# Kernel tuning notes

Hardware: AMD Instinct MI355X
Metric: run time of the kernel (lower is better)

Reference implementation:

```python
import jax, jax.numpy as jnp
import numpy as np

# BD-format field offsets (within 512-dim token vector)
MARK_AX = 0
OP_MUL = 1
OPCODE_BASE = 2          # opcode 27 lives at index OPCODE_BASE + 27
ALU_LO, ALU_HI = 64, 80          # 16-way one-hot nibbles
AX_CARRY_LO, AX_CARRY_HI = 96, 112
OUTPUT_LO, OUTPUT_HI = 128, 144
# GenericE slot layout (within 160-dim GE vector)
NIB_A, NIB_B, RESULT, OP_START = 0, 1, 2, 3
GE_DIM = 160
N_POS = 8
N_LAYERS = 7
OPCODE = 27


def setup_inputs() -> dict:
    key = jax.random.key(0)
    k1, k2, k3 = jax.random.split(key, 3)
    x_bd = jax.random.uniform(k1, (4, 8192, 512), dtype=jnp.float32)
    W = jax.random.normal(k2, (N_LAYERS, GE_DIM, GE_DIM), dtype=jnp.float32) * 0.05
    b = jax.random.normal(k3, (N_LAYERS, GE_DIM), dtype=jnp.float32) * 0.01
    return {"x_bd": x_bd, "W": W, "b": b}


def _decode_nibble(x16):
    # first index k (0..15) with x16[..., k] > 0.5 ; 0.0 if none (matches torch loop)
    return jnp.argmax(x16 > 0.5, axis=-1).astype(x16.dtype)


def reference(x_bd, W, b):
    B, S, D = x_bd.shape
    # active-token mask: both gate bits >= 0.5 (torch code skips if < 0.5)
    mask = (x_bd[..., MARK_AX] >= 0.5) & (x_bd[..., OP_MUL] >= 0.5)  # [B,S]

    # ---- bd_to_ge (vectorized over all tokens) ----
    a_lo = _decode_nibble(x_bd[..., ALU_LO:ALU_LO + 16])
    a_hi = _decode_nibble(x_bd[..., ALU_HI:ALU_HI + 16])
    b_lo = _decode_nibble(x_bd[..., AX_CARRY_LO:AX_CARRY_LO + 16])
    b_hi = _decode_nibble(x_bd[..., AX_CARRY_HI:AX_CARRY_HI + 16])
    op_val = x_bd[..., OPCODE_BASE + OPCODE]  # [B,S]

    x_ge = jnp.zeros((B, S, N_POS, GE_DIM), dtype=x_bd.dtype)
    x_ge = x_ge.at[..., 0, NIB_A].set(a_lo)
    x_ge = x_ge.at[..., 1, NIB_A].set(a_hi)
    x_ge = x_ge.at[..., 0, NIB_B].set(b_lo)
    x_ge = x_ge.at[..., 1, NIB_B].set(b_hi)
    x_ge = x_ge.at[..., :, OP_START + OPCODE].set(op_val[..., None])

    # ---- 7-layer tiny ALU net: Linear(160,160) + ReLU (last layer linear) ----
    h = x_ge
    for i in range(N_LAYERS):
        h = jnp.einsum('bspd,ed->bspe', h, W[i]) + b[i]
        if i < N_LAYERS - 1:
            h = jax.nn.relu(h)

    # ---- ge_to_bd: round, clamp to nibble range, scatter +2.0 one-hots ----
    res_lo = jnp.clip(jnp.round(h[..., 0, RESULT]), 0, 15).astype(jnp.int32)  # [B,S]
    res_hi = jnp.clip(jnp.round(h[..., 1, RESULT]), 0, 15).astype(jnp.int32)
    m = mask[..., None].astype(x_bd.dtype)
    add_lo = 2.0 * jax.nn.one_hot(res_lo, 16, dtype=x_bd.dtype) * m
    add_hi = 2.0 * jax.nn.one_hot(res_hi, 16, dtype=x_bd.dtype) * m

    out = x_bd.at[..., OUTPUT_LO:OUTPUT_LO + 16].add(add_lo)
    out = out.at[..., OUTPUT_HI:OUTPUT_HI + 16].add(add_hi)
    return out
```

## Files before the change

### kernel.cpp

```cpp
#include <hip/hip_runtime.h>
#include <stdint.h>

#define N_TOK 32768
#define TD 512
#define GE 160
#define WSTRIDE (GE * GE)
#define N_MLP_BLK 512
#define N_COPY_BLK 1024
#define HSTR 172

typedef __attribute__((ext_vector_type(8))) short short8;
typedef __attribute__((ext_vector_type(4))) float f32x4;
typedef __attribute__((ext_vector_type(4))) unsigned short us4;

#define OFF_CNT   0
#define OFF_META  256
#define OFF_OPV   (OFF_META + 4 * N_TOK)
#define OFF_L0C   (OFF_OPV + 4 * N_TOK)
#define OFF_WF    (OFF_L0C + 2560 + 256)
#define WS_REQ    (OFF_WF + 250 * 3072)

__device__ __forceinline__ uint32_t nib_first(uint64_t m, int field) {
    uint32_t bits = (uint32_t)((m >> (field * 16)) & 0xFFFFull);
    return bits ? (uint32_t)__builtin_ctz(bits) : 0u;
}
__device__ __forceinline__ unsigned short bf16_rne(float f) {
    uint32_t u = __builtin_bit_cast(uint32_t, f);
    return (unsigned short)((u + 0x7FFFu + ((u >> 16) & 1u)) >> 16);
}
__device__ __forceinline__ float bf16_f(unsigned short h) {
    uint32_t u = ((uint32_t)h) << 16;
    return __builtin_bit_cast(float, u);
}
__device__ __forceinline__ void split3(float v, unsigned short& s1,
                                       unsigned short& s2, unsigned short& s3) {
    s1 = bf16_rne(v); float r  = v - bf16_f(s1);
    s2 = bf16_rne(r); float r2 = r - bf16_f(s2);
    s3 = bf16_rne(r2);
}

__global__ __launch_bounds__(256) void decode_kernel(
        const float* __restrict__ x, const float* __restrict__ W,
        const float* __restrict__ b, uint32_t* __restrict__ cnt,
        uint32_t* __restrict__ meta, float* __restrict__ opv,
        float4* __restrict__ l0c, unsigned short* __restrict__ Wf) {
    const int tid = (int)threadIdx.x;
    if (blockIdx.x < 1024) {
        __shared__ uint32_t l_meta[64];
        __shared__ float    l_opv[64];
        __shared__ uint32_t l_cnt, l_base;
        if (tid == 0) l_cnt = 0;
        __syncthreads();
        const int lane = tid & 63, w = tid >> 6;
        for (int it = 0; it < 8; ++it) {
            int tok = (int)blockIdx.x * 32 + it * 4 + w;
            size_t base = (size_t)tok * TD;
            float nv = x[base + 64 + lane];
            uint64_t m = __ballot(nv > 0.5f);
            if (lane == 0) {
                float g0 = x[base], g1 = x[base + 1];
                if (g0 >= 0.5f && g1 >= 0.5f) {
                    uint32_t idx = atomicAdd(&l_cnt, 1u);
                    l_meta[idx] = (uint32_t)tok | (nib_first(m, 0) << 15) |
                                  (nib_first(m, 1) << 19) | (nib_first(m, 2) << 23) |
                                  (nib_first(m, 3) << 27);
                    l_opv[idx] = x[base + 29];
                }
            }
        }
        __syncthreads();
        if (tid == 0) l_base = atomicAdd(cnt, l_cnt);
        __syncthreads();
        if ((uint32_t)tid < l_cnt) {
            meta[l_base + tid] = l_meta[tid];
            opv[l_base + tid]  = l_opv[tid];
        }
        return;
    }
    int wid = ((int)blockIdx.x - 1024) * 256 + tid;
    if (wid < 16000) {
        int tile = wid >> 6, lane = wid & 63;
        int l = 1 + tile / 50, rem = tile % 50, kt = rem / 10, mt = rem % 10;
        int li = lane & 15, q = lane >> 4;
        const float* src = W + (size_t)l * WSTRIDE + (size_t)(16 * mt + li) * GE +
                           32 * kt + 8 * q;
        short8 A1, A2, A3;
        #pragma unroll
        for (int j = 0; j < 8; ++j) {
            unsigned short s1, s2, s3;
            split3(src[j], s1, s2, s3);
            A1[j] = (short)s1; A2[j] = (short)s2; A3[j] = (short)s3;
        }
        unsigned short* tb = Wf + (size_t)tile * 1536 + lane * 8;
        *(short8*)(tb)        = A1;
        *(short8*)(tb + 512)  = A2;
        *(short8*)(tb + 1024) = A3;
    } else if (wid < 16160) {
        int n = wid - 16000;
        l0c[n] = make_float4(W[(size_t)n * GE + 0], W[(size_t)n * GE + 1],
                             W[(size_t)n * GE + 30], b[n]);
    }
}

__global__ __launch_bounds__(256, 3) void fused_kernel(
        const float* __restrict__ x, const float* __restrict__ W,
        const float* __restrict__ b, float* __restrict__ out,
        const uint32_t* __restrict__ cnt, const uint32_t* __restrict__ meta,
        const float* __restrict__ opv, const float4* __restrict__ l0c,
        const unsigned short* __restrict__ Wf) {
    __shared__ unsigned short hs[3][32][HSTR];
    const int tid = (int)threadIdx.x;

    if (blockIdx.x >= N_MLP_BLK) {
        const int lane = tid & 63, w = tid >> 6;
        int t0 = ((int)blockIdx.x - N_MLP_BLK) * 32 + w * 8;
        const float4* s4 = (const float4*)x;
        float4* d4 = (float4*)out;
        bool gate_lane = (lane >= 32 && lane < 40);
        #pragma unroll
        for (int it = 0; it < 8; ++it) {
            int t = t0 + it;
            size_t fb = (size_t)t * 128;
            float4 v0 = s4[fb + lane];
            float4 v1 = s4[fb + 64 + lane];
            bool skip = false;
            if (gate_lane) {
                float g0 = x[(size_t)t * TD], g1 = x[(size_t)t * TD + 1];
                skip = (g0 >= 0.5f) && (g1 >= 0.5f);
            }
            if (!skip) d4[fb + lane] = v0;
            d4[fb + 64 + lane] = v1;
        }
        return;
    }

    const int lane = tid & 63;
    const int wv   = __builtin_amdgcn_readfirstlane(tid >> 6);
    const int q    = lane >> 4;
    const int li   = lane & 15;
    const int half = lane >> 5, posid = lane & 31;
    const int mstart_tab[4] = {0, 3, 5, 7};
    const int mcnt_tab[4]   = {3, 2, 2, 3};
    const int mystart = mstart_tab[wv], mycnt = mcnt_tab[wv];
    const uint32_t count = *cnt;
    const uint32_t nchunks = (count + 15u) >> 4;

    for (uint32_t ch = blockIdx.x; ch < nchunks; ch += N_MLP_BLK) {
        __syncthreads();

        {
            uint32_t slot0 = ch * 16u + (uint32_t)(posid >> 1);
            float na = 0.f, nb_ = 0.f, op = 0.f;
            if (slot0 < count) {
                uint32_t m = meta[slot0];
                int p = posid & 1;
                na  = (float)((m >> (15 + p * 4)) & 0xFu);
                nb_ = (float)((m >> (23 + p * 4)) & 0xFu);
                op  = opv[slot0];
            }
            #pragma unroll
            for (int g = 0; g < 5; ++g) {
                int nb4 = 40 * wv + 20 * half + 4 * g;
                us4 p1, p2, p3;
                #pragma unroll
                for (int r = 0; r < 4; ++r) {
                    float4 cc = l0c[nb4 + r];
                    float c = cc.w;
                    c = fmaf(cc.x, na, c);
                    c = fmaf(cc.y, nb_, c);
                    c = fmaf(cc.z, op, c);
                    c = fmaxf(c, 0.f);
                    unsigned short s1, s2, s3;
                    split3(c, s1, s2, s3);
                    p1[r] = s1; p2[r] = s2; p3[r] = s3;
                }
                *(us4*)&hs[0][posid][nb4] = p1;
                *(us4*)&hs[1][posid][nb4] = p2;
                *(us4*)&hs[2][posid][nb4] = p3;
            }
        }
        __syncthreads();

        for (int l = 1; l < 6; ++l) {
            const float* bl = b + l * GE;
            f32x4 acc[3][2];
            #pragma unroll
            for (int mi = 0; mi < 3; ++mi)
                #pragma unroll
                for (int nt = 0; nt < 2; ++nt)
                    acc[mi][nt] = (f32x4){0.f, 0.f, 0.f, 0.f};

            for (int kt = 0; kt < 5; ++kt) {
                const int k0 = 32 * kt + 8 * q;
                short8 B1[2], B2[2], B3[2];
                #pragma unroll
                for (int nt = 0; nt < 2; ++nt) {
                    int pos = 16 * nt + li;
                    us4 lo1 = *(const us4*)&hs[0][pos][k0];
                    us4 hi1 = *(const us4*)&hs[0][pos][k0 + 4];
                    us4 lo2 = *(const us4*)&hs[1][pos][k0];
                    us4 hi2 = *(const us4*)&hs[1][pos][k0 + 4];
                    us4 lo3 = *(const us4*)&hs[2][pos][k0];
                    us4 hi3 = *(const us4*)&hs[2][pos][k0 + 4];
                    #pragma unroll
                    for (int j = 0; j < 4; ++j) {
                        B1[nt][j] = (short)lo1[j]; B1[nt][4 + j] = (short)hi1[j];
                        B2[nt][j] = (short)lo2[j]; B2[nt][4 + j] = (short)hi2[j];
                        B3[nt][j] = (short)lo3[j]; B3[nt][4 + j] = (short)hi3[j];
                    }
                }
                #pragma unroll
                for (int mi = 0; mi < 3; ++mi) {
                    if (mi < mycnt) {
                        int mt = mystart + mi;
                        int tidx = ((l - 1) * 5 + kt) * 10 + mt;
                        const unsigned short* tb = Wf + (size_t)tidx * 1536 + lane * 8;
                        short8 A1 = *(const short8*)(tb);
                        short8 A2 = *(const short8*)(tb + 512);
                        short8 A3 = *(const short8*)(tb + 1024);
                        #pragma unroll
                        for (int nt = 0; nt < 2; ++nt) {
                            f32x4 a = acc[mi][nt];
                            a = __builtin_amdgcn_mfma_f32_16x16x32_bf16(A1, B1[nt], a, 0, 0, 0);
                            a = __builtin_amdgcn_mfma_f32_16x16x32_bf16(A1, B2[nt], a, 0, 0, 0);
                            a = __builtin_amdgcn_mfma_f32_16x16x32_bf16(A2, B1[nt], a, 0, 0, 0);
                            a = __builtin_amdgcn_mfma_f32_16x16x32_bf16(A2, B2[nt], a, 0, 0, 0);
                            a = __builtin_amdgcn_mfma_f32_16x16x32_bf16(A1, B3[nt], a, 0, 0, 0);
                            a = __builtin_amdgcn_mfma_f32_16x16x32_bf16(A3, B1[nt], a, 0, 0, 0);
                            acc[mi][nt] = a;
                        }
                    }
                }
            }
            __syncthreads();
            #pragma unroll
            for (int mi = 0; mi < 3; ++mi) {
                if (mi < mycnt) {
                    int nb4 = 16 * (mystart + mi) + 4 * q;
                    #pragma unroll
                    for (int nt = 0; nt < 2; ++nt) {
                        int pos = 16 * nt + li;
                        us4 p1, p2, p3;
                        #pragma unroll
                        for (int r = 0; r < 4; ++r) {
                            float v = fmaxf(acc[mi][nt][r] + bl[nb4 + r], 0.f);
                            unsigned short s1, s2, s3;
                            split3(v, s1, s2, s3);
                            p1[r] = s1; p2[r] = s2; p3[r] = s3;
                        }
                        *(us4*)&hs[0][pos][nb4] = p1;
                        *(us4*)&hs[1][pos][nb4] = p2;
                        *(us4*)&hs[2][pos][nb4] = p3;
                    }
                }
            }
            __syncthreads();
        }

        if (wv == 0) {
            const float* W6 = W + 6 * WSTRIDE + 2 * GE;
            float accp = (half == 0) ? b[6 * GE + 2] : 0.f;
            #pragma unroll
            for (int kb = 0; kb < 10; ++kb) {
                int k0 = 80 * half + 8 * kb;
                us4 a0 = *(const us4*)&hs[0][posid][k0];
                us4 a1 = *(const us4*)&hs[0][posid][k0 + 4];
                us4 b0 = *(const us4*)&hs[1][posid][k0];
                us4 b1 = *(const us4*)&hs[1][posid][k0 + 4];
                us4 c0 = *(const us4*)&hs[2][posid][k0];
                us4 c1 = *(const us4*)&hs[2][posid][k0 + 4];
                const float4* w6f = (const float4*)(W6 + k0);
                float4 w0 = w6f[0], w1 = w6f[1];
                const float* wp0 = (const float*)&w0;
                const float* wp1 = (const float*)&w1;
                #pragma unroll
                for (int j = 0; j < 4; ++j) {
                    float v = (bf16_f(a0[j]) + bf16_f(b0[j])) + bf16_f(c0[j]);
                    accp = fmaf(v, wp0[j], accp);
                }
                #pragma unroll
                for (int j = 0; j < 4; ++j) {
                    float v = (bf16_f(a1[j]) + bf16_f(b1[j])) + bf16_f(c1[j]);
                    accp = fmaf(v, wp1[j], accp);
                }
            }
            float full = accp + __shfl_down(accp, 32);
            int res = (int)fminf(fmaxf(rintf(full), 0.f), 15.f);
            int rhi = __shfl_down(res, 1);
            if (lane < 32 && !(lane & 1)) {
                uint32_t slot = ch * 16u + (uint32_t)(lane >> 1);
                if (slot < count) {
                    int tok = (int)(meta[slot] & 0x7FFFu);
                    const float4* xf = (const float4*)(x + (size_t)tok * TD + 128);
                    float4* of = (float4*)(out + (size_t)tok * TD + 128);
                    int rl = res, rh = 16 + rhi;
                    #pragma unroll
                    for (int i = 0; i < 8; ++i) {
                        float4 v = xf[i];
                        int e = 4 * i;
                        v.x += ((e == rl) || (e == rh)) ? 2.f : 0.f;
                        v.y += ((e + 1 == rl) || (e + 1 == rh)) ? 2.f : 0.f;
                        v.z += ((e + 2 == rl) || (e + 2 == rh)) ? 2.f : 0.f;
                        v.w += ((e + 3 == rl) || (e + 3 == rh)) ? 2.f : 0.f;
                        of[i] = v;
                    }
                }
            }
        }
    }
}

__global__ __launch_bounds__(256) void prep_legacy(
        const float* __restrict__ x, float* __restrict__ out,
        uint32_t* __restrict__ cnt, uint32_t* __restrict__ meta,
        float* __restrict__ opv, int do_compact) {
    __shared__ uint32_t l_meta[64];
    __shared__ float    l_opv[64];
    __shared__ uint32_t l_cnt, l_base;
    const int tid = (int)threadIdx.x;
    if (tid == 0) l_cnt = 0;
    size_t blk = (size_t)blockIdx.x * 4096;
    const float4* s4 = ((const float4*)x) + blk;
    float4*       d4 = ((float4*)out) + blk;
    #pragma unroll
    for (int i = 0; i < 16; ++i) d4[tid + 256 * i] = s4[tid + 256 * i];
    if (!do_compact) return;
    __syncthreads();
    const int lane = tid & 63, w = tid >> 6;
    for (int it = 0; it < 8; ++it) {
        int tok = (int)blockIdx.x * 32 + it * 4 + w;
        size_t base = (size_t)tok * TD;
        float nv = x[base + 64 + lane];
        uint64_t m = __ballot(nv > 0.5f);
        if (lane == 0) {
            float g0 = x[base], g1 = x[base + 1];
            if (g0 >= 0.5f && g1 >= 0.5f) {
                uint32_t idx = atomicAdd(&l_cnt, 1u);
                l_meta[idx] = (uint32_t)tok | (nib_first(m, 0) << 15) |
                              (nib_first(m, 1) << 19) | (nib_first(m, 2) << 23) |
                              (nib_first(m, 3) << 27);
                l_opv[idx] = x[base + 29];
            }
        }
    }
    __syncthreads();
    if (tid == 0) l_base = atomicAdd(cnt, l_cnt);
    __syncthreads();
    if ((uint32_t)tid < l_cnt) {
        meta[l_base + tid] = l_meta[tid];
        opv[l_base + tid]  = l_opv[tid];
    }
}

template <bool COMPACT>
__global__ __launch_bounds__(1024) void mlp_legacy(
        const float* __restrict__ x, const float* __restrict__ W,
        const float* __restrict__ b, float* __restrict__ out,
        const uint32_t* __restrict__ cnt, const uint32_t* __restrict__ meta,
        const float* __restrict__ opv) {
    __shared__ float h[GE][64];
    const int lane = (int)(threadIdx.x & 63u);
    const int w    = __builtin_amdgcn_readfirstlane((int)(threadIdx.x >> 6));
    const int p    = lane & 1;
    const uint32_t count   = COMPACT ? *cnt : (uint32_t)N_TOK;
    const uint32_t nchunks = (count + 31u) >> 5;
    for (uint32_t ch = blockIdx.x; ch < nchunks; ch += gridDim.x) {
        uint32_t slot = ch * 32u + (uint32_t)(lane >> 1);
        bool active = slot < count;
        int tok = 0;
        float na = 0.f, nb = 0.f, op = 0.f;
        if (COMPACT) {
            if (active) {
                uint32_t mt = meta[slot];
                tok = (int)(mt & 0x7FFFu);
                uint32_t nib = mt >> 15;
                na = (float)((nib >> (p * 4)) & 0xFu);
                nb = (float)((nib >> (8 + p * 4)) & 0xFu);
                op = opv[slot];
            }
        } else {
            tok = (int)slot;
            if (active) {
                size_t tb = (size_t)tok * TD;
                float g0 = x[tb], g1 = x[tb + 1];
                active = (g0 >= 0.5f) && (g1 >= 0.5f);
                if (active) {
                    const float* ap = x + tb + 64 + 16 * p;
                    const float* bp = x + tb + 96 + 16 * p;
                    #pragma unroll
                    for (int i = 15; i >= 0; --i) { if (ap[i] > 0.5f) na = (float)i; }
                    #pragma unroll
                    for (int i = 15; i >= 0; --i) { if (bp[i] > 0.5f) nb = (float)i; }
                    op = x[tb + 29];
                }
            }
        }
        float c[10];
        {
            #pragma unroll
            for (int j = 0; j < 10; ++j) {
                int n = 10 * w + j;
                float cc = b[n];
                cc = fmaf(W[n * GE + 0],  na, cc);
                cc = fmaf(W[n * GE + 1],  nb, cc);
                cc = fmaf(W[n * GE + 30], op, cc);
                c[j] = fmaxf(cc, 0.f);
            }
        }
        __syncthreads();
        #pragma unroll
        for (int j = 0; j < 10; ++j) h[10 * w + j][lane] = c[j];
        __syncthreads();
        for (int l = 1; l < 6; ++l) {
            const float* Wl = W + l * WSTRIDE;
            const float* bl = b + l * GE;
            #pragma unroll
            for (int j = 0; j < 10; ++j) c[j] = bl[10 * w + j];
            for (int k0 = 0; k0 < GE; k0 += 16) {
                float hr[16];
                #pragma unroll
                for (int kk = 0; kk < 16; ++kk) hr[kk] = h[k0 + kk][lane];
                #pragma unroll
                for (int j = 0; j < 10; ++j) {
                    const float* wr = Wl + (10 * w + j) * GE + k0;
                    #pragma unroll
                    for (int kk = 0; kk < 16; ++kk)
                        c[j] = fmaf(hr[kk], wr[kk], c[j]);
                }
            }
            __syncthreads();
            #pragma unroll
            for (int j = 0; j < 10; ++j)
                h[10 * w + j][lane] = fmaxf(c[j], 0.f);
            __syncthreads();
        }
        if (w == 0) {
            const float* W6 = W + 6 * WSTRIDE + 2 * GE;
            float acc = b[6 * GE + 2];
            #pragma unroll 16
            for (int k = 0; k < GE; ++k) acc = fmaf(h[k][lane], W6[k], acc);
            if (active) {
                float r = rintf(acc);
                r = fminf(fmaxf(r, 0.f), 15.f);
                int res = (int)r;
                out[(size_t)tok * TD + 128 + 16 * p + res] += 2.0f;
            }
        }
    }
}

extern "C" void kernel_launch(void* const* d_in, const int* in_sizes, int n_in,
                              void* d_out, int out_size, void* d_ws, size_t ws_size,
                              hipStream_t stream) {
    const float* x = (const float*)d_in[0];
    const float* W = (const float*)d_in[1];
    const float* b = (const float*)d_in[2];
    float* out = (float*)d_out;

    uint32_t* cnt  = (uint32_t*)((char*)d_ws + OFF_CNT);
    uint32_t* meta = (uint32_t*)((char*)d_ws + OFF_META);
    float*    opv  = (float*)((char*)d_ws + OFF_OPV);
    float4*   l0c  = (float4*)((char*)d_ws + OFF_L0C);
    unsigned short* Wf = (unsigned short*)((char*)d_ws + OFF_WF);

    if (ws_size >= (size_t)WS_REQ) {
        hipMemsetAsync(d_ws, 0, 4, stream);
        decode_kernel<<<1024 + 64, 256, 0, stream>>>(x, W, b, cnt, meta, opv,
                                                     l0c, Wf);
        fused_kernel<<<N_MLP_BLK + N_COPY_BLK, 256, 0, stream>>>(
            x, W, b, out, cnt, meta, opv, l0c, Wf);
    } else {
        bool compact = ws_size >= (size_t)(256 + 8 * (size_t)N_TOK);
        if (compact) hipMemsetAsync(d_ws, 0, 4, stream);
        prep_legacy<<<N_TOK / 32, 256, 0, stream>>>(x, out, cnt, meta, opv,
                                                    compact ? 1 : 0);
        if (compact)
            mlp_legacy<true><<<512, 1024, 0, stream>>>(x, W, b, out, cnt, meta, opv);
        else
            mlp_legacy<false><<<512, 1024, 0, stream>>>(x, W, b, out, cnt, meta, opv);
    }
}
```

Before: 172.2 us.

## Replace compaction pipeline with dense per-block fused copy+MLP mega kernel

Removes the memset, the decode/compaction pass and the atomic counter. Each block now handles 16 consecutive tokens: it copies them, decodes the gate and nibbles into shared memory, and runs the MFMA MLP on all 16 tokens whether they are active or not. This drops one kernel launch and the separate metadata traffic, and reads x only once for both the copy and the decode. In exchange the MLP runs on every token instead of only the masked ones, which adds compute when few tokens are active.

```diff
diff --git a/kernel.cpp b/kernel.cpp
--- a/kernel.cpp
+++ b/kernel.cpp
@@ -5,20 +5,18 @@
 #define TD 512
 #define GE 160
 #define WSTRIDE (GE * GE)
-#define N_MLP_BLK 512
-#define N_COPY_BLK 1024
 #define HSTR 172
 
 typedef __attribute__((ext_vector_type(8))) short short8;
 typedef __attribute__((ext_vector_type(4))) float f32x4;
 typedef __attribute__((ext_vector_type(4))) unsigned short us4;
 
-#define OFF_CNT   0
-#define OFF_META  256
-#define OFF_OPV   (OFF_META + 4 * N_TOK)
-#define OFF_L0C   (OFF_OPV + 4 * N_TOK)
-#define OFF_WF    (OFF_L0C + 2560 + 256)
+#define OFF_L0C   0
+#define OFF_WF    2816
 #define WS_REQ    (OFF_WF + 250 * 3072)
+#define LOFF_CNT  0
+#define LOFF_META 256
+#define LOFF_OPV  (LOFF_META + 4 * N_TOK)
 
 __device__ __forceinline__ uint32_t nib_first(uint64_t m, int field) {
     uint32_t bits = (uint32_t)((m >> (field * 16)) & 0xFFFFull);
@@ -39,45 +37,10 @@
     s3 = bf16_rne(r2);
 }
 
-__global__ __launch_bounds__(256) void decode_kernel(
-        const float* __restrict__ x, const float* __restrict__ W,
-        const float* __restrict__ b, uint32_t* __restrict__ cnt,
-        uint32_t* __restrict__ meta, float* __restrict__ opv,
+__global__ __launch_bounds__(256) void wprep_kernel(
+        const float* __restrict__ W, const float* __restrict__ b,
         float4* __restrict__ l0c, unsigned short* __restrict__ Wf) {
-    const int tid = (int)threadIdx.x;
-    if (blockIdx.x < 1024) {
-        __shared__ uint32_t l_meta[64];
-        __shared__ float    l_opv[64];
-        __shared__ uint32_t l_cnt, l_base;
-        if (tid == 0) l_cnt = 0;
-        __syncthreads();
-        const int lane = tid & 63, w = tid >> 6;
-        for (int it = 0; it < 8; ++it) {
-            int tok = (int)blockIdx.x * 32 + it * 4 + w;
-            size_t base = (size_t)tok * TD;
-            float nv = x[base + 64 + lane];
-            uint64_t m = __ballot(nv > 0.5f);
-            if (lane == 0) {
-                float g0 = x[base], g1 = x[base + 1];
-                if (g0 >= 0.5f && g1 >= 0.5f) {
-                    uint32_t idx = atomicAdd(&l_cnt, 1u);
-                    l_meta[idx] = (uint32_t)tok | (nib_first(m, 0) << 15) |
-                                  (nib_first(m, 1) << 19) | (nib_first(m, 2) << 23) |
-                                  (nib_first(m, 3) << 27);
-                    l_opv[idx] = x[base + 29];
-                }
-            }
-        }
-        __syncthreads();
-        if (tid == 0) l_base = atomicAdd(cnt, l_cnt);
-        __syncthreads();
-        if ((uint32_t)tid < l_cnt) {
-            meta[l_base + tid] = l_meta[tid];
-            opv[l_base + tid]  = l_opv[tid];
-        }
-        return;
-    }
-    int wid = ((int)blockIdx.x - 1024) * 256 + tid;
+    int wid = (int)blockIdx.x * 256 + (int)threadIdx.x;
     if (wid < 16000) {
         int tile = wid >> 6, lane = wid & 63;
         int l = 1 + tile / 50, rem = tile % 50, kt = rem / 10, mt = rem % 10;
@@ -102,208 +65,210 @@
     }
 }
 
-__global__ __launch_bounds__(256, 3) void fused_kernel(
+__global__ __launch_bounds__(256, 4) void mega_kernel(
         const float* __restrict__ x, const float* __restrict__ W,
         const float* __restrict__ b, float* __restrict__ out,
-        const uint32_t* __restrict__ cnt, const uint32_t* __restrict__ meta,
-        const float* __restrict__ opv, const float4* __restrict__ l0c,
-        const unsigned short* __restrict__ Wf) {
+        const float4* __restrict__ l0c, const unsigned short* __restrict__ Wf) {
     __shared__ unsigned short hs[3][32][HSTR];
-    const int tid = (int)threadIdx.x;
-
-    if (blockIdx.x >= N_MLP_BLK) {
-        const int lane = tid & 63, w = tid >> 6;
-        int t0 = ((int)blockIdx.x - N_MLP_BLK) * 32 + w * 8;
-        const float4* s4 = (const float4*)x;
-        float4* d4 = (float4*)out;
-        bool gate_lane = (lane >= 32 && lane < 40);
-        #pragma unroll
-        for (int it = 0; it < 8; ++it) {
-            int t = t0 + it;
-            size_t fb = (size_t)t * 128;
-            float4 v0 = s4[fb + lane];
-            float4 v1 = s4[fb + 64 + lane];
-            bool skip = false;
-            if (gate_lane) {
-                float g0 = x[(size_t)t * TD], g1 = x[(size_t)t * TD + 1];
-                skip = (g0 >= 0.5f) && (g1 >= 0.5f);
-            }
-            if (!skip) d4[fb + lane] = v0;
-            d4[fb + 64 + lane] = v1;
-        }
-        return;
-    }
-
+    __shared__ uint32_t nibs[16];
+    __shared__ float    opx[16];
+    __shared__ uint32_t actarr[16];
+
+    const int tid  = (int)threadIdx.x;
     const int lane = tid & 63;
     const int wv   = __builtin_amdgcn_readfirstlane(tid >> 6);
     const int q    = lane >> 4;
     const int li   = lane & 15;
     const int half = lane >> 5, posid = lane & 31;
+    const int t0   = (int)blockIdx.x * 16;
+
+    float4 cp[8];
+    const float4* s4 = (const float4*)x + (size_t)blockIdx.x * 2048;
+    #pragma unroll
+    for (int i = 0; i < 8; ++i) cp[i] = s4[tid + 256 * i];
+
+    #pragma unroll
+    for (int it = 0; it < 4; ++it) {
+        int tl = wv * 4 + it;
+        size_t base = (size_t)(t0 + tl) * TD;
+        float nv = x[base + 64 + lane];
+        uint64_t m = __ballot(nv > 0.5f);
+        if (lane == 0) {
+            float g0 = x[base], g1 = x[base + 1];
+            actarr[tl] = (g0 >= 0.5f && g1 >= 0.5f) ? 1u : 0u;
+            nibs[tl] = nib_first(m, 0) | (nib_first(m, 1) << 4) |
+                       (nib_first(m, 2) << 8) | (nib_first(m, 3) << 12);
+            opx[tl] = x[base + 29];
+        }
+    }
+    __syncthreads();
+
+    {
+        float4* d4 = (float4*)out + (size_t)blockIdx.x * 2048;
+        #pragma unroll
+        for (int i = 0; i < 8; ++i) {
+            int f4 = tid + 256 * i;
+            int tl = f4 >> 7, w = f4 & 127;
+            bool skip = (w >= 32) && (w < 40) && (actarr[tl] != 0u);
+            if (!skip) d4[f4] = cp[i];
+        }
+    }
+
+    {
+        int tl = posid >> 1, p = posid & 1;
+        uint32_t nib = nibs[tl];
+        float na  = (float)((nib >> (4 * p)) & 0xFu);
+        float nb_ = (float)((nib >> (8 + 4 * p)) & 0xFu);
+        float op  = opx[tl];
+        #pragma unroll
+        for (int g = 0; g < 5; ++g) {
+            int nb4 = 40 * wv + 20 * half + 4 * g;
+            us4 p1, p2, p3;
+            #pragma unroll
+            for (int r = 0; r < 4; ++r) {
+                float4 cc = l0c[nb4 + r];
+                float c = cc.w;
+                c = fmaf(cc.x, na, c);
+                c = fmaf(cc.y, nb_, c);
+                c = fmaf(cc.z, op, c);
+                c = fmaxf(c, 0.f);
+                unsigned short s1, s2, s3;
+                split3(c, s1, s2, s3);
+                p1[r] = s1; p2[r] = s2; p3[r] = s3;
+            }
+            *(us4*)&hs[0][posid][nb4] = p1;
+            *(us4*)&hs[1][posid][nb4] = p2;
+            *(us4*)&hs[2][posid][nb4] = p3;
+        }
+    }
+    __syncthreads();
+
     const int mstart_tab[4] = {0, 3, 5, 7};
     const int mcnt_tab[4]   = {3, 2, 2, 3};
     const int mystart = mstart_tab[wv], mycnt = mcnt_tab[wv];
-    const uint32_t count = *cnt;
-    const uint32_t nchunks = (count + 15u) >> 4;
-
-    for (uint32_t ch = blockIdx.x; ch < nchunks; ch += N_MLP_BLK) {
+
+    for (int l = 1; l < 6; ++l) {
+        const float* bl = b + l * GE;
+        f32x4 acc[3][2];
+        #pragma unroll
+        for (int mi = 0; mi < 3; ++mi)
+            #pragma unroll
+            for (int nt = 0; nt < 2; ++nt)
+                acc[mi][nt] = (f32x4){0.f, 0.f, 0.f, 0.f};
+
+        for (int kt = 0; kt < 5; ++kt) {
+            const int k0 = 32 * kt + 8 * q;
+            short8 B1[2], B2[2], B3[2];
+            #pragma unroll
+            for (int nt = 0; nt < 2; ++nt) {
+                int pos = 16 * nt + li;
+                us4 lo1 = *(const us4*)&hs[0][pos][k0];
+                us4 hi1 = *(const us4*)&hs[0][pos][k0 + 4];
+                us4 lo2 = *(const us4*)&hs[1][pos][k0];
+                us4 hi2 = *(const us4*)&hs[1][pos][k0 + 4];
+                us4 lo3 = *(const us4*)&hs[2][pos][k0];
+                us4 hi3 = *(const us4*)&hs[2][pos][k0 + 4];
+                #pragma unroll
+                for (int j = 0; j < 4; ++j) {
+                    B1[nt][j] = (short)lo1[j]; B1[nt][4 + j] = (short)hi1[j];
+                    B2[nt][j] = (short)lo2[j]; B2[nt][4 + j] = (short)hi2[j];
+                    B3[nt][j] = (short)lo3[j]; B3[nt][4 + j] = (short)hi3[j];
+                }
+            }
+            #pragma unroll
+            for (int mi = 0; mi < 3; ++mi) {
+                if (mi < mycnt) {
+                    int mt = mystart + mi;
+                    int tidx = ((l - 1) * 5 + kt) * 10 + mt;
+                    const unsigned short* tb = Wf + (size_t)tidx * 1536 + lane * 8;
+                    short8 A1 = *(const short8*)(tb);
+                    short8 A2 = *(const short8*)(tb + 512);
+                    short8 A3 = *(const short8*)(tb + 1024);
+                    #pragma unroll
+                    for (int nt = 0; nt < 2; ++nt) {
+                        f32x4 a = acc[mi][nt];
+                        a = __builtin_amdgcn_mfma_f32_16x16x32_bf16(A1, B1[nt], a, 0, 0, 0);
+                        a = __builtin_amdgcn_mfma_f32_16x16x32_bf16(A1, B2[nt], a, 0, 0, 0);
+                        a = __builtin_amdgcn_mfma_f32_16x16x32_bf16(A2, B1[nt], a, 0, 0, 0);
+                        a = __builtin_amdgcn_mfma_f32_16x16x32_bf16(A2, B2[nt], a, 0, 0, 0);
+                        a = __builtin_amdgcn_mfma_f32_16x16x32_bf16(A1, B3[nt], a, 0, 0, 0);
+                        a = __builtin_amdgcn_mfma_f32_16x16x32_bf16(A3, B1[nt], a, 0, 0, 0);
+                        acc[mi][nt] = a;
+                    }
+                }
+            }
+        }
         __syncthreads();
-
-        {
-            uint32_t slot0 = ch * 16u + (uint32_t)(posid >> 1);
-            float na = 0.f, nb_ = 0.f, op = 0.f;
-            if (slot0 < count) {
-                uint32_t m = meta[slot0];
-                int p = posid & 1;
-                na  = (float)((m >> (15 + p * 4)) & 0xFu);
-                nb_ = (float)((m >> (23 + p * 4)) & 0xFu);
-                op  = opv[slot0];
-            }
-            #pragma unroll
-            for (int g = 0; g < 5; ++g) {
-                int nb4 = 40 * wv + 20 * half + 4 * g;
-                us4 p1, p2, p3;
-                #pragma unroll
-                for (int r = 0; r < 4; ++r) {
-                    float4 cc = l0c[nb4 + r];
-                    float c = cc.w;
-                    c = fmaf(cc.x, na, c);
-                    c = fmaf(cc.y, nb_, c);
-                    c = fmaf(cc.z, op, c);
-                    c = fmaxf(c, 0.f);
-                    unsigned short s1, s2, s3;
-                    split3(c, s1, s2, s3);
-                    p1[r] = s1; p2[r] = s2; p3[r] = s3;
-                }
-                *(us4*)&hs[0][posid][nb4] = p1;
-                *(us4*)&hs[1][posid][nb4] = p2;
-                *(us4*)&hs[2][posid][nb4] = p3;
-            }
-        }
-        __syncthreads();
-
-        for (int l = 1; l < 6; ++l) {
-            const float* bl = b + l * GE;
-            f32x4 acc[3][2];
-            #pragma unroll
-            for (int mi = 0; mi < 3; ++mi)
-                #pragma unroll
-                for (int nt = 0; nt < 2; ++nt)
-                    acc[mi][nt] = (f32x4){0.f, 0.f, 0.f, 0.f};
-
-            for (int kt = 0; kt < 5; ++kt) {
-                const int k0 = 32 * kt + 8 * q;
-                short8 B1[2], B2[2], B3[2];
+        #pragma unroll
+        for (int mi = 0; mi < 3; ++mi) {
+            if (mi < mycnt) {
+                int nb4 = 16 * (mystart + mi) + 4 * q;
                 #pragma unroll
                 for (int nt = 0; nt < 2; ++nt) {
                     int pos = 16 * nt + li;
-                    us4 lo1 = *(const us4*)&hs[0][pos][k0];
-                    us4 hi1 = *(const us4*)&hs[0][pos][k0 + 4];
-                    us4 lo2 = *(const us4*)&hs[1][pos][k0];
-                    us4 hi2 = *(const us4*)&hs[1][pos][k0 + 4];
-                    us4 lo3 = *(const us4*)&hs[2][pos][k0];
-                    us4 hi3 = *(const us4*)&hs[2][pos][k0 + 4];
+                    us4 p1, p2, p3;
                     #pragma unroll
-                    for (int j = 0; j < 4; ++j) {
-                        B1[nt][j] = (short)lo1[j]; B1[nt][4 + j] = (short)hi1[j];
-                        B2[nt][j] = (short)lo2[j]; B2[nt][4 + j] = (short)hi2[j];
-                        B3[nt][j] = (short)lo3[j]; B3[nt][4 + j] = (short)hi3[j];
+                    for (int r = 0; r < 4; ++r) {
+                        float v = fmaxf(acc[mi][nt][r] + bl[nb4 + r], 0.f);
+                        unsigned short s1, s2, s3;
+                        split3(v, s1, s2, s3);
+                        p1[r] = s1; p2[r] = s2; p3[r] = s3;
                     }
-                }
+                    *(us4*)&hs[0][pos][nb4] = p1;
+                    *(us4*)&hs[1][pos][nb4] = p2;
+                    *(us4*)&hs[2][pos][nb4] = p3;
+                }
+            }
+        }
+        __syncthreads();
+    }
+
+    if (wv == 0) {
+        const float* W6 = W + 6 * WSTRIDE + 2 * GE;
+        float accp = (half == 0) ? b[6 * GE + 2] : 0.f;
+        #pragma unroll
+        for (int kb = 0; kb < 10; ++kb) {
+            int k0 = 80 * half + 8 * kb;
+            us4 a0 = *(const us4*)&hs[0][posid][k0];
+            us4 a1 = *(const us4*)&hs[0][posid][k0 + 4];
+            us4 b0 = *(const us4*)&hs[1][posid][k0];
+            us4 b1 = *(const us4*)&hs[1][posid][k0 + 4];
+            us4 c0 = *(const us4*)&hs[2][posid][k0];
+            us4 c1 = *(const us4*)&hs[2][posid][k0 + 4];
+            const float4* w6f = (const float4*)(W6 + k0);
+            float4 w0 = w6f[0], w1 = w6f[1];
+            const float* wp0 = (const float*)&w0;
+            const float* wp1 = (const float*)&w1;
+            #pragma unroll
+            for (int j = 0; j < 4; ++j) {
+                float v = (bf16_f(a0[j]) + bf16_f(b0[j])) + bf16_f(c0[j]);
+                accp = fmaf(v, wp0[j], accp);
+            }
+            #pragma unroll
+            for (int j = 0; j < 4; ++j) {
+                float v = (bf16_f(a1[j]) + bf16_f(b1[j])) + bf16_f(c1[j]);
+                accp = fmaf(v, wp1[j], accp);
+            }
+        }
+        float full = accp + __shfl_down(accp, 32);
+        int res = (int)fminf(fmaxf(rintf(full), 0.f), 15.f);
+        int rhi = __shfl_down(res, 1);
+        if (lane < 32 && !(lane & 1)) {
+            int tl = lane >> 1;
+            if (actarr[tl] != 0u) {
+                int tok = t0 + tl;
+                const float4* xf = (const float4*)(x + (size_t)tok * TD + 128);
+                float4* of = (float4*)(out + (size_t)tok * TD + 128);
+                int rl = res, rh = 16 + rhi;
                 #pragma unroll
-                for (int mi = 0; mi < 3; ++mi) {
-                    if (mi < mycnt) {
-                        int mt = mystart + mi;
-                        int tidx = ((l - 1) * 5 + kt) * 10 + mt;
-                        const unsigned short* tb = Wf + (size_t)tidx * 1536 + lane * 8;
-                        short8 A1 = *(const short8*)(tb);
-                        short8 A2 = *(const short8*)(tb + 512);
-                        short8 A3 = *(const short8*)(tb + 1024);
-                        #pragma unroll
-                        for (int nt = 0; nt < 2; ++nt) {
-                            f32x4 a = acc[mi][nt];
-                            a = __builtin_amdgcn_mfma_f32_16x16x32_bf16(A1, B1[nt], a, 0, 0, 0);
-                            a = __builtin_amdgcn_mfma_f32_16x16x32_bf16(A1, B2[nt], a, 0, 0, 0);
-                            a = __builtin_amdgcn_mfma_f32_16x16x32_bf16(A2, B1[nt], a, 0, 0, 0);
-                            a = __builtin_amdgcn_mfma_f32_16x16x32_bf16(A2, B2[nt], a, 0, 0, 0);
-                            a = __builtin_amdgcn_mfma_f32_16x16x32_bf16(A1, B3[nt], a, 0, 0, 0);
-                            a = __builtin_amdgcn_mfma_f32_16x16x32_bf16(A3, B1[nt], a, 0, 0, 0);
-                            acc[mi][nt] = a;
-                        }
-                    }
-                }
-            }
-            __syncthreads();
-            #pragma unroll
-            for (int mi = 0; mi < 3; ++mi) {
-                if (mi < mycnt) {
-                    int nb4 = 16 * (mystart + mi) + 4 * q;
-                    #pragma unroll
-                    for (int nt = 0; nt < 2; ++nt) {
-                        int pos = 16 * nt + li;
-                        us4 p1, p2, p3;
-                        #pragma unroll
-                        for (int r = 0; r < 4; ++r) {
-                            float v = fmaxf(acc[mi][nt][r] + bl[nb4 + r], 0.f);
-                            unsigned short s1, s2, s3;
-                            split3(v, s1, s2, s3);
-                            p1[r] = s1; p2[r] = s2; p3[r] = s3;
-                        }
-                        *(us4*)&hs[0][pos][nb4] = p1;
-                        *(us4*)&hs[1][pos][nb4] = p2;
-                        *(us4*)&hs[2][pos][nb4] = p3;
-                    }
-                }
-            }
-            __syncthreads();
-        }
-
-        if (wv == 0) {
-            const float* W6 = W + 6 * WSTRIDE + 2 * GE;
-            float accp = (half == 0) ? b[6 * GE + 2] : 0.f;
-            #pragma unroll
-            for (int kb = 0; kb < 10; ++kb) {
-                int k0 = 80 * half + 8 * kb;
-                us4 a0 = *(const us4*)&hs[0][posid][k0];
-                us4 a1 = *(const us4*)&hs[0][posid][k0 + 4];
-                us4 b0 = *(const us4*)&hs[1][posid][k0];
-                us4 b1 = *(const us4*)&hs[1][posid][k0 + 4];
-                us4 c0 = *(const us4*)&hs[2][posid][k0];
-                us4 c1 = *(const us4*)&hs[2][posid][k0 + 4];
-                const float4* w6f = (const float4*)(W6 + k0);
-                float4 w0 = w6f[0], w1 = w6f[1];
-                const float* wp0 = (const float*)&w0;
-                const float* wp1 = (const float*)&w1;
-                #pragma unroll
-                for (int j = 0; j < 4; ++j) {
-                    float v = (bf16_f(a0[j]) + bf16_f(b0[j])) + bf16_f(c0[j]);
-                    accp = fmaf(v, wp0[j], accp);
-                }
-                #pragma unroll
-                for (int j = 0; j < 4; ++j) {
-                    float v = (bf16_f(a1[j]) + bf16_f(b1[j])) + bf16_f(c1[j]);
-                    accp = fmaf(v, wp1[j], accp);
-                }
-            }
-            float full = accp + __shfl_down(accp, 32);
-            int res = (int)fminf(fmaxf(rintf(full), 0.f), 15.f);
-            int rhi = __shfl_down(res, 1);
-            if (lane < 32 && !(lane & 1)) {
-                uint32_t slot = ch * 16u + (uint32_t)(lane >> 1);
-                if (slot < count) {
-                    int tok = (int)(meta[slot] & 0x7FFFu);
-                    const float4* xf = (const float4*)(x + (size_t)tok * TD + 128);
-                    float4* of = (float4*)(out + (size_t)tok * TD + 128);
-                    int rl = res, rh = 16 + rhi;
-                    #pragma unroll
-                    for (int i = 0; i < 8; ++i) {
-                        float4 v = xf[i];
-                        int e = 4 * i;
-                        v.x += ((e == rl) || (e == rh)) ? 2.f : 0.f;
-                        v.y += ((e + 1 == rl) || (e + 1 == rh)) ? 2.f : 0.f;
-                        v.z += ((e + 2 == rl) || (e + 2 == rh)) ? 2.f : 0.f;
-                        v.w += ((e + 3 == rl) || (e + 3 == rh)) ? 2.f : 0.f;
-                        of[i] = v;
-                    }
+                for (int i = 0; i < 8; ++i) {
+                    float4 v = xf[i];
+                    int e = 4 * i;
+                    v.x += ((e == rl) || (e == rh)) ? 2.f : 0.f;
+                    v.y += ((e + 1 == rl) || (e + 1 == rh)) ? 2.f : 0.f;
+                    v.z += ((e + 2 == rl) || (e + 2 == rh)) ? 2.f : 0.f;
+                    v.w += ((e + 3 == rl) || (e + 3 == rh)) ? 2.f : 0.f;
+                    of[i] = v;
                 }
             }
         }
@@ -457,19 +422,15 @@
     const float* b = (const float*)d_in[2];
     float* out = (float*)d_out;
 
-    uint32_t* cnt  = (uint32_t*)((char*)d_ws + OFF_CNT);
-    uint32_t* meta = (uint32_t*)((char*)d_ws + OFF_META);
-    float*    opv  = (float*)((char*)d_ws + OFF_OPV);
-    float4*   l0c  = (float4*)((char*)d_ws + OFF_L0C);
-    unsigned short* Wf = (unsigned short*)((char*)d_ws + OFF_WF);
-
     if (ws_size >= (size_t)WS_REQ) {
-        hipMemsetAsync(d_ws, 0, 4, stream);
-        decode_kernel<<<1024 + 64, 256, 0, stream>>>(x, W, b, cnt, meta, opv,
-                                                     l0c, Wf);
-        fused_kernel<<<N_MLP_BLK + N_COPY_BLK, 256, 0, stream>>>(
-            x, W, b, out, cnt, meta, opv, l0c, Wf);
+        float4* l0c = (float4*)((char*)d_ws + OFF_L0C);
+        unsigned short* Wf = (unsigned short*)((char*)d_ws + OFF_WF);
+        wprep_kernel<<<64, 256, 0, stream>>>(W, b, l0c, Wf);
+        mega_kernel<<<N_TOK / 16, 256, 0, stream>>>(x, W, b, out, l0c, Wf);
     } else {
+        uint32_t* cnt  = (uint32_t*)((char*)d_ws + LOFF_CNT);
+        uint32_t* meta = (uint32_t*)((char*)d_ws + LOFF_META);
+        float*    opv  = (float*)((char*)d_ws + LOFF_OPV);
         bool compact = ws_size >= (size_t)(256 + 8 * (size_t)N_TOK);
         if (compact) hipMemsetAsync(d_ws, 0, 4, stream);
         prep_legacy<<<N_TOK / 32, 256, 0, stream>>>(x, out, cnt, meta, opv,
```

Result: slower. 226.2 us (+31.4%).
